# Performance work log

Measured on AMD Instinct MI355X. Metric: run time of the kernel, lower is better.

Reference implementation:

```python
import jax, jax.numpy as jnp
import numpy as np

K = 5       # kernel_size
UP = 2      # up_factor
EPS = 1e-5  # BatchNorm eps (eval mode)


def _conv(x, w, pad, dil=1):
    return jax.lax.conv_general_dilated(
        x, w, (1, 1), [(pad, pad), (pad, pad)], rhs_dilation=(dil, dil),
        dimension_numbers=('NCHW', 'OIHW', 'NCHW'))


def _bn(x, g, b, m, v):
    inv = g / jnp.sqrt(v + EPS)
    return x * inv[:, None, None] + (b - m * inv)[:, None, None]


def _bilinear(x, oh, ow):
    # torch F.interpolate(mode='bilinear', align_corners=False)
    N, C, H, W = x.shape
    def coords(out_s, in_s):
        s = in_s / out_s
        src = (jnp.arange(out_s, dtype=jnp.float32) + 0.5) * s - 0.5
        src = jnp.clip(src, 0.0, in_s - 1)
        i0 = jnp.floor(src).astype(jnp.int32)
        i1 = jnp.minimum(i0 + 1, in_s - 1)
        return i0, i1, src - i0
    y0, y1, wy = coords(oh, H)
    x0, x1, wx = coords(ow, W)
    g = lambda yi, xi: x[:, :, yi][:, :, :, xi]  # (N,C,oh,ow)
    top = g(y0, x0) * (1 - wx) + g(y0, x1) * wx
    bot = g(y1, x0) * (1 - wx) + g(y1, x1) * wx
    return top * (1 - wy)[:, None] + bot * wy[:, None]


def _unfold(x):
    # F.unfold(k=5, pad=2) reshaped to (N, C, K*K, H, W); channel-major (c, kh, kw)
    p = K // 2
    N, C, H, W = x.shape
    xp = jnp.pad(x, ((0, 0), (0, 0), (p, p), (p, p)))
    patches = [xp[:, :, i:i + H, j:j + W] for i in range(K) for j in range(K)]
    return jnp.stack(patches, axis=2)


def setup_inputs() -> dict:
    key = jax.random.key(0)
    ks = jax.random.split(key, 8)
    N, C, H, W = 2, 256, 48, 48
    Cc = C // 4
    Cout = 256
    d = {}
    d['x'] = jax.random.normal(ks[0], (N, C, H, W), dtype=jnp.float32)
    d['compress_w'] = jax.random.normal(ks[1], (Cc, C, 1, 1), dtype=jnp.float32) * 0.05
    d['g1'] = jnp.ones((Cc,), jnp.float32)
    d['b1'] = jnp.zeros((Cc,), jnp.float32)
    d['m1'] = jax.random.normal(ks[2], (Cc,), dtype=jnp.float32) * 0.1
    d['v1'] = jax.random.uniform(ks[3], (Cc,), minval=0.5, maxval=1.5, dtype=jnp.float32)
    d['ke1_w'] = jax.random.normal(ks[4], (Cc, Cc, 3, 3), dtype=jnp.float32) * 0.05
    d['gk'] = jnp.ones((Cc,), jnp.float32)
    d['bk'] = jnp.zeros((Cc,), jnp.float32)
    d['mk'] = jax.random.normal(ks[5], (Cc,), dtype=jnp.float32) * 0.1
    d['vk'] = jax.random.uniform(ks[6], (Cc,), minval=0.5, maxval=1.5, dtype=jnp.float32)
    d['ke2_w'] = jax.random.normal(ks[7], (UP * UP * K * K, Cc, 3, 3), dtype=jnp.float32) * 0.05
    d['proj_w'] = jax.random.normal(jax.random.fold_in(key, 10), (Cout, C, 1, 1), dtype=jnp.float32) * 0.05
    d['g2'] = jnp.ones((Cout,), jnp.float32)
    d['b2'] = jnp.zeros((Cout,), jnp.float32)
    d['m2'] = jax.random.normal(jax.random.fold_in(key, 11), (Cout,), dtype=jnp.float32) * 0.1
    d['v2'] = jax.random.uniform(jax.random.fold_in(key, 12), (Cout,), minval=0.5, maxval=1.5, dtype=jnp.float32)
    return d


def reference(x, compress_w, g1, b1, m1, v1, ke1_w, gk, bk, mk, vk, ke2_w,
              proj_w, g2, b2, m2, v2):
    N, C, H, W = x.shape
    oh, ow = H * UP, W * UP
    # kernel prediction branch
    comp = jax.nn.relu(_bn(_conv(x, compress_w, 0), g1, b1, m1, v1))
    k1 = jax.nn.relu(_bn(_conv(comp, ke1_w, 2, dil=2), gk, bk, mk, vk))
    kernel = _conv(k1, ke2_w, 1)                               # (N, UP^2*K^2, H, W)
    kernel = jax.nn.softmax(kernel.reshape(N, UP * UP, K * K, H, W), axis=2)
    # content reassembly
    x_up = jnp.repeat(jnp.repeat(x, UP, axis=2), UP, axis=3)
    x_unf = _unfold(x_up)                                      # (N, C, K^2, oh, ow)
    k_up = _bilinear(kernel.reshape(N, UP * UP * K * K, H, W), oh, ow)
    k_up = k_up.reshape(N, UP * UP, K * K, oh, ow)
    out = jnp.einsum('nckhw,nukhw->nuchw', x_unf, k_up)        # (N, UP^2, C, oh, ow)
    # view (N, UP^2*C, oh, ow) then pixel_shuffle(UP)
    out = out.reshape(N, UP * UP * C, oh, ow)
    out = out.reshape(N, C, UP, UP, oh, ow)
    out = out.transpose(0, 1, 4, 2, 5, 3).reshape(N, C, oh * UP, ow * UP)
    out = jax.nn.relu(_bn(_conv(out, proj_w, 0), g2, b2, m2, v2))
    return out
```

## Files before the change

kernel.cpp:

```cpp
#include <hip/hip_runtime.h>

#define EPSB 1e-5f

typedef __attribute__((ext_vector_type(8))) short bf16x8;
typedef __attribute__((ext_vector_type(4))) float f32x4;

__device__ __forceinline__ unsigned short f2b(float f) {
  union { float f; unsigned u; } cv; cv.f = f;
  unsigned r = cv.u + 0x7FFFu + ((cv.u >> 16) & 1u);
  return (unsigned short)(r >> 16);
}

__global__ __launch_bounds__(256) void k_compress(
    const float* __restrict__ x, const float* __restrict__ cw,
    const float* __restrict__ g1, const float* __restrict__ b1,
    const float* __restrict__ m1, const float* __restrict__ v1,
    const float* __restrict__ k1w, const float* __restrict__ k2w,
    const float* __restrict__ pw,
    unsigned short* __restrict__ comp_t, unsigned short* __restrict__ k1_t,
    unsigned short* __restrict__ pwb, unsigned short* __restrict__ wt1,
    unsigned short* __restrict__ wt2) {
  int bid = blockIdx.x, t = threadIdx.x;
  if (bid >= 96) {
    int u = (bid - 96) * 256 + t;
    if (u < 65536) {
      pwb[u] = f2b(pw[u]);
    } else if (u < 102400) {
      int a = u - 65536;
      int co = a / 576, k = a % 576, tap = k >> 6, ci = k & 63;
      wt1[a] = f2b(k1w[co * 576 + ci * 9 + tap]);
    } else if (u < 176128) {
      int c2 = u - 102400;
      int co = c2 / 576, k = c2 % 576, tap = k >> 6, ci = k & 63;
      wt2[c2] = (co < 100) ? f2b(k2w[co * 576 + ci * 9 + tap]) : (unsigned short)0;
    } else {
      int v = u - 176128;
      if (v < 25600) {
        int n = v / 12800, r = v % 12800;
        int bp = r >> 5, c32 = r & 31;
        int rr, cc;
        if (bp < 104) { rr = bp / 52; cc = bp % 52; }
        else if (bp >= 296) { rr = 50 + (bp - 296) / 52; cc = (bp - 296) % 52; }
        else { int q = bp - 104; rr = 2 + (q >> 2); int c4 = q & 3; cc = (c4 < 2) ? c4 : c4 + 48; }
        ((unsigned*)comp_t)[((size_t)n * 2704 + rr * 52 + cc) * 32 + c32] = 0u;
      } else if (v < 38144) {
        int j = v - 25600;
        int n = j / 6272, r = j % 6272;
        int bp = r >> 5, c32 = r & 31;
        int rr, cc;
        if (bp < 50) { rr = 0; cc = bp; }
        else if (bp >= 146) { rr = 49; cc = bp - 146; }
        else { int q = bp - 50; rr = 1 + (q >> 1); cc = (q & 1) * 49; }
        ((unsigned*)k1_t)[((size_t)n * 2500 + rr * 50 + cc) * 32 + c32] = 0u;
      }
    }
    return;
  }
  __shared__ __align__(16) unsigned short wlds[16384];
  __shared__ __align__(16) unsigned short xlds[12288];
  int n = bid / 48, y = bid % 48;
  for (int f = t; f < 16384; f += 256) {
    int co = f >> 8, ci = f & 255;
    int ba = (f * 2) ^ ((co & 7) << 4);
    *(unsigned short*)((char*)wlds + ba) = f2b(cw[f]);
  }
  const float* xrow = x + (size_t)n * 256 * 2304 + y * 48;
  for (int f = t; f < 12288; f += 256) {
    int ci = f / 48, px = f - ci * 48;
    int ba = ((px * 256 + ci) * 2) ^ ((px & 7) << 4);
    *(unsigned short*)((char*)xlds + ba) = f2b(xrow[(size_t)ci * 2304 + px]);
  }
  __syncthreads();
  int wid = t >> 6, l = t & 63, l15 = l & 15, lg = l >> 4;
  f32x4 acc[3];
  acc[0] = acc[1] = acc[2] = (f32x4){0.f, 0.f, 0.f, 0.f};
  int coA = wid * 16 + l15;
#pragma unroll
  for (int kbi = 0; kbi < 8; ++kbi) {
    int col = kbi * 32 + lg * 8;
    bf16x8 afr = *(const bf16x8*)((char*)wlds + (((coA * 256 + col) * 2) ^ ((coA & 7) << 4)));
#pragma unroll
    for (int nt = 0; nt < 3; ++nt) {
      int px = nt * 16 + l15;
      bf16x8 bfr = *(const bf16x8*)((char*)xlds + (((px * 256 + col) * 2) ^ ((px & 7) << 4)));
      acc[nt] = __builtin_amdgcn_mfma_f32_16x16x32_bf16(afr, bfr, acc[nt], 0, 0, 0);
    }
  }
  int co0 = wid * 16 + lg * 4;
  float s0 = g1[co0] / sqrtf(v1[co0] + EPSB);
  float s1 = g1[co0 + 1] / sqrtf(v1[co0 + 1] + EPSB);
  float s2 = g1[co0 + 2] / sqrtf(v1[co0 + 2] + EPSB);
  float s3 = g1[co0 + 3] / sqrtf(v1[co0 + 3] + EPSB);
  float d0 = b1[co0] - m1[co0] * s0;
  float d1 = b1[co0 + 1] - m1[co0 + 1] * s1;
  float d2 = b1[co0 + 2] - m1[co0 + 2] * s2;
  float d3 = b1[co0 + 3] - m1[co0 + 3] * s3;
  unsigned short* dst = comp_t + ((size_t)n * 2704 + (y + 2) * 52) * 64;
#pragma unroll
  for (int nt = 0; nt < 3; ++nt) {
    int px = nt * 16 + l15;
    ushort4 pk;
    pk.x = f2b(fmaxf(fmaf(acc[nt][0], s0, d0), 0.f));
    pk.y = f2b(fmaxf(fmaf(acc[nt][1], s1, d1), 0.f));
    pk.z = f2b(fmaxf(fmaf(acc[nt][2], s2, d2), 0.f));
    pk.w = f2b(fmaxf(fmaf(acc[nt][3], s3, d3), 0.f));
    *(ushort4*)&dst[(px + 2) * 64 + co0] = pk;
  }
}

__global__ __launch_bounds__(128) void k_ke1(
    const unsigned short* __restrict__ comp_t, const unsigned short* __restrict__ wt1,
    const float* __restrict__ gk, const float* __restrict__ bk,
    const float* __restrict__ mk, const float* __restrict__ vk,
    unsigned short* __restrict__ k1_t) {
  __shared__ unsigned short sA[16640];
  int bid = blockIdx.x, t = threadIdx.x;
  int n = bid / 96, rem = bid % 96;
  int y = rem >> 1, coh = rem & 1;
  const unsigned short* src = comp_t + ((size_t)n * 52 + y) * 52 * 64;
  for (int f = t; f < 2080; f += 128) {
    int g = f >> 3, ci0 = (f & 7) * 8;
    int cc = g % 52, rr = g / 52;
    bf16x8 vv = *(const bf16x8*)&src[(rr * 52 + cc) * 64 + ci0];
    int ba = (((rr * 52 + cc) * 64 + ci0) * 2) ^ ((cc & 7) << 4);
    *(bf16x8*)((char*)sA + ba) = vv;
  }
  __syncthreads();
  int wid = t >> 6, l = t & 63, l15 = l & 15, lg = l >> 4;
  f32x4 acc[3];
  acc[0] = acc[1] = acc[2] = (f32x4){0.f, 0.f, 0.f, 0.f};
  const unsigned short* arow = wt1 + (size_t)(coh * 32 + wid * 16 + l15) * 576;
#pragma unroll
  for (int kbi = 0; kbi < 18; ++kbi) {
    int tap = kbi >> 1;
    int ky = tap / 3, kx = tap % 3;
    int ci0 = (kbi & 1) * 32 + lg * 8;
    bf16x8 afr = *(const bf16x8*)&arow[kbi * 32 + lg * 8];
#pragma unroll
    for (int nt = 0; nt < 3; ++nt) {
      int col = nt * 16 + l15 + 2 * kx;
      int ba = (((2 * ky * 52 + col) * 64 + ci0) * 2) ^ ((col & 7) << 4);
      bf16x8 bfr = *(const bf16x8*)((char*)sA + ba);
      acc[nt] = __builtin_amdgcn_mfma_f32_16x16x32_bf16(afr, bfr, acc[nt], 0, 0, 0);
    }
  }
  unsigned short* dst = k1_t + ((size_t)n * 50 + (y + 1)) * 50 * 64;
  int co0 = coh * 32 + wid * 16 + lg * 4;
  float s0 = gk[co0] / sqrtf(vk[co0] + EPSB);
  float s1 = gk[co0 + 1] / sqrtf(vk[co0 + 1] + EPSB);
  float s2 = gk[co0 + 2] / sqrtf(vk[co0 + 2] + EPSB);
  float s3 = gk[co0 + 3] / sqrtf(vk[co0 + 3] + EPSB);
  float d0 = bk[co0] - mk[co0] * s0;
  float d1 = bk[co0 + 1] - mk[co0 + 1] * s1;
  float d2 = bk[co0 + 2] - mk[co0 + 2] * s2;
  float d3 = bk[co0 + 3] - mk[co0 + 3] * s3;
#pragma unroll
  for (int nt = 0; nt < 3; ++nt) {
    int px = nt * 16 + l15;
    ushort4 pk;
    pk.x = f2b(fmaxf(fmaf(acc[nt][0], s0, d0), 0.f));
    pk.y = f2b(fmaxf(fmaf(acc[nt][1], s1, d1), 0.f));
    pk.z = f2b(fmaxf(fmaf(acc[nt][2], s2, d2), 0.f));
    pk.w = f2b(fmaxf(fmaf(acc[nt][3], s3, d3), 0.f));
    *(ushort4*)&dst[(px + 1) * 64 + co0] = pk;
  }
}

__global__ __launch_bounds__(128) void k_ke2(
    const unsigned short* __restrict__ k1_t, const unsigned short* __restrict__ wt2,
    float* __restrict__ kern_t) {
  __shared__ unsigned short sA[9600];
  int bid = blockIdx.x, t = threadIdx.x;
  int n = bid / 96, rem = bid % 96;
  int y = rem >> 1, coh = rem & 1;
  const unsigned short* src = k1_t + ((size_t)n * 50 + y) * 50 * 64;
  for (int f = t; f < 1200; f += 128) {
    int g = f >> 3, ci0 = (f & 7) * 8;
    int cc = g % 50, rr = g / 50;
    bf16x8 vv = *(const bf16x8*)&src[(rr * 50 + cc) * 64 + ci0];
    int ba = (((rr * 50 + cc) * 64 + ci0) * 2) ^ ((cc & 7) << 4);
    *(bf16x8*)((char*)sA + ba) = vv;
  }
  __syncthreads();
  int wid = t >> 6, l = t & 63, l15 = l & 15, lg = l >> 4;
  f32x4 acc[2][3];
#pragma unroll
  for (int mi = 0; mi < 2; ++mi)
#pragma unroll
    for (int nt = 0; nt < 3; ++nt) acc[mi][nt] = (f32x4){0.f, 0.f, 0.f, 0.f};
#pragma unroll
  for (int kbi = 0; kbi < 18; ++kbi) {
    int tap = kbi >> 1;
    int ky = tap / 3, kx = tap % 3;
    int ci0 = (kbi & 1) * 32 + lg * 8;
    bf16x8 afr[2];
#pragma unroll
    for (int mi = 0; mi < 2; ++mi)
      afr[mi] = *(const bf16x8*)&wt2[(size_t)(coh * 64 + (wid * 2 + mi) * 16 + l15) * 576 + kbi * 32 + lg * 8];
#pragma unroll
    for (int nt = 0; nt < 3; ++nt) {
      int col = nt * 16 + l15 + kx;
      int ba = (((ky * 50 + col) * 64 + ci0) * 2) ^ ((col & 7) << 4);
      bf16x8 bfr = *(const bf16x8*)((char*)sA + ba);
      acc[0][nt] = __builtin_amdgcn_mfma_f32_16x16x32_bf16(afr[0], bfr, acc[0][nt], 0, 0, 0);
      acc[1][nt] = __builtin_amdgcn_mfma_f32_16x16x32_bf16(afr[1], bfr, acc[1][nt], 0, 0, 0);
    }
  }
#pragma unroll
  for (int mi = 0; mi < 2; ++mi) {
    int co0 = coh * 64 + (wid * 2 + mi) * 16 + lg * 4;
    if (co0 < 112) {
#pragma unroll
      for (int nt = 0; nt < 3; ++nt) {
        int px = nt * 16 + l15;
        float4 vv = {acc[mi][nt][0], acc[mi][nt][1], acc[mi][nt][2], acc[mi][nt][3]};
        *(float4*)&kern_t[((size_t)n * 2304 + y * 48 + px) * 112 + co0] = vv;
      }
    }
  }
}

__global__ __launch_bounds__(512, 4) void k_fused(
    const float* __restrict__ x, const float* __restrict__ kern_t,
    const unsigned short* __restrict__ pwb,
    const float* __restrict__ g2, const float* __restrict__ b2,
    const float* __restrict__ m2, const float* __restrict__ v2,
    float* __restrict__ out) {
  __shared__ __align__(16) char smem[76800];
  float* xls  = (float*)smem;
  float* w9s  = (float*)(smem + 35840);
  float* sb2s = (float*)(smem + 40448);
  unsigned short* finT = (unsigned short*)(smem + 44032);
  float* ks   = (float*)(smem + 44032);

  int blk = blockIdx.x;
  int n = blk / 288, r = blk % 288;
  int y48 = r / 6, xt = r % 6;
  int X0 = xt * 32, x480 = xt * 8;
  int t = threadIdx.x;

  if (t < 256) {
    float iv = g2[t] / sqrtf(v2[t] + EPSB);
    sb2s[t] = iv; sb2s[256 + t] = b2[t] - m2[t] * iv;
  }
  for (int f = t; f < 840; f += 512) {
    int slot = f / 280, rem = f % 280;
    int cx = rem / 28, c4 = rem % 28;
    int sy = min(max(y48 + slot - 1, 0), 47);
    int sx = min(max(x480 + cx - 1, 0), 47);
    float4 vv = *(const float4*)&kern_t[((size_t)n * 2304 + sy * 48 + sx) * 112 + c4 * 4];
    *(float4*)&ks[(slot * 10 + cx) * 112 + c4 * 4] = vv;
  }
  const float* xb = x + (size_t)n * 256 * 2304;
  for (int f = t; f < 8448; f += 512) {
    int c = f / 33, rc = f - c * 33;
    int ry = rc / 11, cx = rc - ry * 11;
    int sy = min(max(y48 + ry - 1, 0), 47);
    int sx = min(max(x480 + cx - 1, 0), 47);
    int slot = (c & 3) * 64 + (c >> 2);
    xls[slot * 35 + rc] = xb[(size_t)c * 2304 + sy * 48 + sx];
  }
  __syncthreads();

  {
    int s = t & 3, tri = t >> 2;
    int u = tri & 3, w2l = (tri >> 2) & 15, yhh = tri >> 6;
    int y96 = 2 * y48 + yhh;
    int w2 = xt * 16 + w2l;
    float syf = fminf(fmaxf(y96 * 0.5f - 0.25f, 0.f), 47.f);
    int y0 = (int)syf; float wy = syf - (float)y0; int y1 = min(y0 + 1, 47);
    float sxf = fminf(fmaxf(w2 * 0.5f - 0.25f, 0.f), 47.f);
    int x0 = (int)sxf; float wx = sxf - (float)x0; int x1 = min(x0 + 1, 47);
    int slr = ((s & 2) ? y1 : y0) - y48 + 1;
    int cxr = ((s & 1) ? x1 : x0) - x480 + 1;
    float wgt = ((s & 1) ? wx : 1.f - wx) * ((s & 2) ? wy : 1.f - wy);
    const float* p = &ks[(slr * 10 + cxr) * 112 + u * 25];
    float bl[25], mx = -3.4e38f;
#pragma unroll
    for (int k = 0; k < 25; ++k) { bl[k] = p[k]; mx = fmaxf(mx, bl[k]); }
    float sum = 0.f;
#pragma unroll
    for (int k = 0; k < 25; ++k) { bl[k] = __expf(bl[k] - mx); sum += bl[k]; }
    float rs = wgt / sum;
#pragma unroll
    for (int k = 0; k < 25; ++k) {
      bl[k] *= rs;
      bl[k] += __shfl_xor(bl[k], 1);
      bl[k] += __shfl_xor(bl[k], 2);
    }
    if (s == 0) {
#pragma unroll
      for (int kh = 0; kh < 5; ++kh) {
        bool vy = (unsigned)(y96 + kh - 2) < 96u;
#pragma unroll
        for (int kw = 0; kw < 5; ++kw) {
          bool vx = (unsigned)(w2 + kw - 2) < 96u;
          if (!(vy && vx)) bl[kh * 5 + kw] = 0.f;
        }
      }
      int py = yhh, px_ = w2l & 1;
      float cc0[5], cc1[5], cc2[5];
#pragma unroll
      for (int kh = 0; kh < 5; ++kh) {
        cc0[kh] = px_ ? bl[kh * 5 + 0] : bl[kh * 5 + 0] + bl[kh * 5 + 1];
        cc1[kh] = px_ ? bl[kh * 5 + 1] + bl[kh * 5 + 2] : bl[kh * 5 + 2] + bl[kh * 5 + 3];
        cc2[kh] = px_ ? bl[kh * 5 + 3] + bl[kh * 5 + 4] : bl[kh * 5 + 4];
      }
      float* op = &w9s[(yhh * 16 + w2l) * 36 + u * 9];
      op[0] = py ? cc0[0] : cc0[0] + cc0[1];
      op[1] = py ? cc1[0] : cc1[0] + cc1[1];
      op[2] = py ? cc2[0] : cc2[0] + cc2[1];
      op[3] = py ? cc0[1] + cc0[2] : cc0[2] + cc0[3];
      op[4] = py ? cc1[1] + cc1[2] : cc1[2] + cc1[3];
      op[5] = py ? cc2[1] + cc2[2] : cc2[2] + cc2[3];
      op[6] = py ? cc0[3] + cc0[4] : cc0[4];
      op[7] = py ? cc1[3] + cc1[4] : cc1[4];
      op[8] = py ? cc2[3] + cc2[4] : cc2[4];
    }
  }
  __syncthreads();

  int ci = t & 255, rY = t >> 8;
  int u = ci >> 6, ch = ci & 63;
  int cb = ci >> 3, crr = ci & 7;
  int wid = t >> 6, l = t & 63, l15 = l & 15, lg = l >> 4;
  const unsigned short* a0p = pwb + (size_t)(wid * 32 + l15) * 256;
  const unsigned short* a1p = a0p + 16 * 256;
  size_t outn = (size_t)n * 256 * 36864;
  int Ybase = 4 * y48;

#pragma unroll
  for (int c = 0; c < 2; ++c) {
    {
      const float* xc0 = &xls[((rY * 2 + 0) * 64 + ch) * 35];
      const float* xc1 = &xls[((rY * 2 + 1) * 64 + ch) * 35];
      float xw0[9], xw1[9];
#pragma unroll
      for (int ry = 0; ry < 3; ++ry)
#pragma unroll
        for (int cx = 0; cx < 3; ++cx) {
          xw0[ry * 3 + cx] = xc0[ry * 11 + cx];
          xw1[ry * 3 + cx] = xc1[ry * 11 + cx];
        }
#pragma unroll
      for (int j = 0; j < 16; ++j) {
        if (j >= 2 && (j & 1) == 0) {
          int nc = (j >> 1) + 2;
#pragma unroll
          for (int ry = 0; ry < 3; ++ry) {
            xw0[ry*3+0]=xw0[ry*3+1]; xw0[ry*3+1]=xw0[ry*3+2]; xw0[ry*3+2]=xc0[ry*11+nc];
            xw1[ry*3+0]=xw1[ry*3+1]; xw1[ry*3+1]=xw1[ry*3+2]; xw1[ry*3+2]=xc1[ry*11+nc];
          }
        }
        const float* wt = &w9s[(c * 16 + j) * 36 + u * 9];
        float a0 = 0.f, a1 = 0.f;
#pragma unroll
        for (int k9 = 0; k9 < 9; ++k9) {
          float wv = wt[k9];
          a0 = fmaf(xw0[k9], wv, a0);
          a1 = fmaf(xw1[k9], wv, a1);
        }
        int px0 = rY * 32 + 2 * j, px1 = px0 + 1;
        finT[px0 * 256 + ((cb ^ (px0 & 7)) * 8 + crr)] = f2b(a0);
        finT[px1 * 256 + ((cb ^ (px1 & 7)) * 8 + crr)] = f2b(a1);
      }
    }
    __syncthreads();

    f32x4 acc[2][4];
#pragma unroll
    for (int mi = 0; mi < 2; ++mi)
#pragma unroll
      for (int nt = 0; nt < 4; ++nt) acc[mi][nt] = (f32x4){0.f, 0.f, 0.f, 0.f};
#pragma unroll
    for (int kbi = 0; kbi < 8; ++kbi) {
      bf16x8 afr0 = *(const bf16x8*)&a0p[kbi * 32 + lg * 8];
      bf16x8 afr1 = *(const bf16x8*)&a1p[kbi * 32 + lg * 8];
      int cbk = kbi * 4 + lg;
#pragma unroll
      for (int nt = 0; nt < 4; ++nt) {
        int row = nt * 16 + l15;
        bf16x8 bfr = *(const bf16x8*)&finT[row * 256 + ((cbk ^ (row & 7)) * 8)];
        acc[0][nt] = __builtin_amdgcn_mfma_f32_16x16x32_bf16(afr0, bfr, acc[0][nt], 0, 0, 0);
        acc[1][nt] = __builtin_amdgcn_mfma_f32_16x16x32_bf16(afr1, bfr, acc[1][nt], 0, 0, 0);
      }
    }
#pragma unroll
    for (int mi = 0; mi < 2; ++mi) {
#pragma unroll
      for (int r4 = 0; r4 < 4; ++r4) {
        int o = (wid * 2 + mi) * 16 + lg * 4 + r4;
        float sc = sb2s[o], bi = sb2s[256 + o];
#pragma unroll
        for (int nt = 0; nt < 4; ++nt) {
          int px = nt * 16 + l15;
          int Yl = c * 2 + (px >> 5), Xl = px & 31;
          float val = fmaxf(fmaf(acc[mi][nt][r4], sc, bi), 0.f);
          out[outn + (size_t)o * 36864 + (size_t)(Ybase + Yl) * 192 + X0 + Xl] = val;
        }
      }
    }
    if (c == 0) __syncthreads();
  }
}

extern "C" void kernel_launch(void* const* d_in, const int* in_sizes, int n_in,
                              void* d_out, int out_size, void* d_ws, size_t ws_size,
                              hipStream_t stream) {
  const float* x   = (const float*)d_in[0];
  const float* cw  = (const float*)d_in[1];
  const float* g1  = (const float*)d_in[2];
  const float* b1  = (const float*)d_in[3];
  const float* m1  = (const float*)d_in[4];
  const float* v1  = (const float*)d_in[5];
  const float* k1w = (const float*)d_in[6];
  const float* gk  = (const float*)d_in[7];
  const float* bk  = (const float*)d_in[8];
  const float* mk  = (const float*)d_in[9];
  const float* vk  = (const float*)d_in[10];
  const float* k2w = (const float*)d_in[11];
  const float* pw  = (const float*)d_in[12];
  const float* g2  = (const float*)d_in[13];
  const float* b2  = (const float*)d_in[14];
  const float* m2  = (const float*)d_in[15];
  const float* v2  = (const float*)d_in[16];
  float* out = (float*)d_out;
  float* ws  = (float*)d_ws;

  unsigned short* comp_t = (unsigned short*)ws;
  unsigned short* k1_t   = (unsigned short*)(ws + 173056);
  float* kern_t = ws + 333056;
  unsigned short* pwb = (unsigned short*)(ws + 849152);
  unsigned short* wt1 = (unsigned short*)(ws + 881920);
  unsigned short* wt2 = (unsigned short*)(ws + 900352);

  k_compress<<<933, 256, 0, stream>>>(x, cw, g1, b1, m1, v1, k1w, k2w, pw,
                                      comp_t, k1_t, pwb, wt1, wt2);
  k_ke1<<<192, 128, 0, stream>>>(comp_t, wt1, gk, bk, mk, vk, k1_t);
  k_ke2<<<192, 128, 0, stream>>>(k1_t, wt2, kern_t);
  k_fused<<<576, 512, 0, stream>>>(x, kern_t, pwb, g2, b2, m2, v2, out);
}
```

Before: 185.9 us.

## Fuse ke1 and ke2 convolutions into main kernel with halo recompute

Removes the separate ke1 and ke2 kernels and their global intermediates. Each block of the fused kernel now computes the dilated 3x3 conv and the kernel-prediction conv for its own tile plus a halo from comp_t in shared memory, then proceeds to reassembly and projection. The x tile is also staged as bf16 instead of fp32 to reduce shared memory use. This saves two launches and global round trips, at the cost of redundant halo compute (each block recomputes overlapping k1 and kernel values) and lower precision on x.

```diff
diff --git a/kernel.cpp b/kernel.cpp
--- a/kernel.cpp
+++ b/kernel.cpp
@@ -9,6 +9,10 @@
   union { float f; unsigned u; } cv; cv.f = f;
   unsigned r = cv.u + 0x7FFFu + ((cv.u >> 16) & 1u);
   return (unsigned short)(r >> 16);
+}
+__device__ __forceinline__ float b2f(unsigned short v) {
+  union { unsigned u; float f; } cv; cv.u = ((unsigned)v) << 16;
+  return cv.f;
 }
 
 __global__ __launch_bounds__(256) void k_compress(
@@ -17,9 +21,8 @@
     const float* __restrict__ m1, const float* __restrict__ v1,
     const float* __restrict__ k1w, const float* __restrict__ k2w,
     const float* __restrict__ pw,
-    unsigned short* __restrict__ comp_t, unsigned short* __restrict__ k1_t,
-    unsigned short* __restrict__ pwb, unsigned short* __restrict__ wt1,
-    unsigned short* __restrict__ wt2) {
+    unsigned short* __restrict__ comp_t, unsigned short* __restrict__ pwb,
+    unsigned short* __restrict__ wt1, unsigned short* __restrict__ wt2) {
   int bid = blockIdx.x, t = threadIdx.x;
   if (bid >= 96) {
     int u = (bid - 96) * 256 + t;
@@ -43,15 +46,6 @@
         else if (bp >= 296) { rr = 50 + (bp - 296) / 52; cc = (bp - 296) % 52; }
         else { int q = bp - 104; rr = 2 + (q >> 2); int c4 = q & 3; cc = (c4 < 2) ? c4 : c4 + 48; }
         ((unsigned*)comp_t)[((size_t)n * 2704 + rr * 52 + cc) * 32 + c32] = 0u;
-      } else if (v < 38144) {
-        int j = v - 25600;
-        int n = j / 6272, r = j % 6272;
-        int bp = r >> 5, c32 = r & 31;
-        int rr, cc;
-        if (bp < 50) { rr = 0; cc = bp; }
-        else if (bp >= 146) { rr = 49; cc = bp - 146; }
-        else { int q = bp - 50; rr = 1 + (q >> 1); cc = (q & 1) * 49; }
-        ((unsigned*)k1_t)[((size_t)n * 2500 + rr * 50 + cc) * 32 + c32] = 0u;
       }
     }
     return;
@@ -60,7 +54,7 @@
   __shared__ __align__(16) unsigned short xlds[12288];
   int n = bid / 48, y = bid % 48;
   for (int f = t; f < 16384; f += 256) {
-    int co = f >> 8, ci = f & 255;
+    int co = f >> 8;
     int ba = (f * 2) ^ ((co & 7) << 4);
     *(unsigned short*)((char*)wlds + ba) = f2b(cw[f]);
   }
@@ -108,148 +102,51 @@
   }
 }
 
-__global__ __launch_bounds__(128) void k_ke1(
-    const unsigned short* __restrict__ comp_t, const unsigned short* __restrict__ wt1,
+__global__ __launch_bounds__(512, 4) void k_mega(
+    const float* __restrict__ x, const unsigned short* __restrict__ comp_t,
+    const unsigned short* __restrict__ wt1, const unsigned short* __restrict__ wt2,
+    const unsigned short* __restrict__ pwb,
     const float* __restrict__ gk, const float* __restrict__ bk,
     const float* __restrict__ mk, const float* __restrict__ vk,
-    unsigned short* __restrict__ k1_t) {
-  __shared__ unsigned short sA[16640];
-  int bid = blockIdx.x, t = threadIdx.x;
-  int n = bid / 96, rem = bid % 96;
-  int y = rem >> 1, coh = rem & 1;
-  const unsigned short* src = comp_t + ((size_t)n * 52 + y) * 52 * 64;
-  for (int f = t; f < 2080; f += 128) {
-    int g = f >> 3, ci0 = (f & 7) * 8;
-    int cc = g % 52, rr = g / 52;
-    bf16x8 vv = *(const bf16x8*)&src[(rr * 52 + cc) * 64 + ci0];
-    int ba = (((rr * 52 + cc) * 64 + ci0) * 2) ^ ((cc & 7) << 4);
-    *(bf16x8*)((char*)sA + ba) = vv;
-  }
-  __syncthreads();
-  int wid = t >> 6, l = t & 63, l15 = l & 15, lg = l >> 4;
-  f32x4 acc[3];
-  acc[0] = acc[1] = acc[2] = (f32x4){0.f, 0.f, 0.f, 0.f};
-  const unsigned short* arow = wt1 + (size_t)(coh * 32 + wid * 16 + l15) * 576;
-#pragma unroll
-  for (int kbi = 0; kbi < 18; ++kbi) {
-    int tap = kbi >> 1;
-    int ky = tap / 3, kx = tap % 3;
-    int ci0 = (kbi & 1) * 32 + lg * 8;
-    bf16x8 afr = *(const bf16x8*)&arow[kbi * 32 + lg * 8];
-#pragma unroll
-    for (int nt = 0; nt < 3; ++nt) {
-      int col = nt * 16 + l15 + 2 * kx;
-      int ba = (((2 * ky * 52 + col) * 64 + ci0) * 2) ^ ((col & 7) << 4);
-      bf16x8 bfr = *(const bf16x8*)((char*)sA + ba);
-      acc[nt] = __builtin_amdgcn_mfma_f32_16x16x32_bf16(afr, bfr, acc[nt], 0, 0, 0);
-    }
-  }
-  unsigned short* dst = k1_t + ((size_t)n * 50 + (y + 1)) * 50 * 64;
-  int co0 = coh * 32 + wid * 16 + lg * 4;
-  float s0 = gk[co0] / sqrtf(vk[co0] + EPSB);
-  float s1 = gk[co0 + 1] / sqrtf(vk[co0 + 1] + EPSB);
-  float s2 = gk[co0 + 2] / sqrtf(vk[co0 + 2] + EPSB);
-  float s3 = gk[co0 + 3] / sqrtf(vk[co0 + 3] + EPSB);
-  float d0 = bk[co0] - mk[co0] * s0;
-  float d1 = bk[co0 + 1] - mk[co0 + 1] * s1;
-  float d2 = bk[co0 + 2] - mk[co0 + 2] * s2;
-  float d3 = bk[co0 + 3] - mk[co0 + 3] * s3;
-#pragma unroll
-  for (int nt = 0; nt < 3; ++nt) {
-    int px = nt * 16 + l15;
-    ushort4 pk;
-    pk.x = f2b(fmaxf(fmaf(acc[nt][0], s0, d0), 0.f));
-    pk.y = f2b(fmaxf(fmaf(acc[nt][1], s1, d1), 0.f));
-    pk.z = f2b(fmaxf(fmaf(acc[nt][2], s2, d2), 0.f));
-    pk.w = f2b(fmaxf(fmaf(acc[nt][3], s3, d3), 0.f));
-    *(ushort4*)&dst[(px + 1) * 64 + co0] = pk;
-  }
-}
-
-__global__ __launch_bounds__(128) void k_ke2(
-    const unsigned short* __restrict__ k1_t, const unsigned short* __restrict__ wt2,
-    float* __restrict__ kern_t) {
-  __shared__ unsigned short sA[9600];
-  int bid = blockIdx.x, t = threadIdx.x;
-  int n = bid / 96, rem = bid % 96;
-  int y = rem >> 1, coh = rem & 1;
-  const unsigned short* src = k1_t + ((size_t)n * 50 + y) * 50 * 64;
-  for (int f = t; f < 1200; f += 128) {
-    int g = f >> 3, ci0 = (f & 7) * 8;
-    int cc = g % 50, rr = g / 50;
-    bf16x8 vv = *(const bf16x8*)&src[(rr * 50 + cc) * 64 + ci0];
-    int ba = (((rr * 50 + cc) * 64 + ci0) * 2) ^ ((cc & 7) << 4);
-    *(bf16x8*)((char*)sA + ba) = vv;
-  }
-  __syncthreads();
-  int wid = t >> 6, l = t & 63, l15 = l & 15, lg = l >> 4;
-  f32x4 acc[2][3];
-#pragma unroll
-  for (int mi = 0; mi < 2; ++mi)
-#pragma unroll
-    for (int nt = 0; nt < 3; ++nt) acc[mi][nt] = (f32x4){0.f, 0.f, 0.f, 0.f};
-#pragma unroll
-  for (int kbi = 0; kbi < 18; ++kbi) {
-    int tap = kbi >> 1;
-    int ky = tap / 3, kx = tap % 3;
-    int ci0 = (kbi & 1) * 32 + lg * 8;
-    bf16x8 afr[2];
-#pragma unroll
-    for (int mi = 0; mi < 2; ++mi)
-      afr[mi] = *(const bf16x8*)&wt2[(size_t)(coh * 64 + (wid * 2 + mi) * 16 + l15) * 576 + kbi * 32 + lg * 8];
-#pragma unroll
-    for (int nt = 0; nt < 3; ++nt) {
-      int col = nt * 16 + l15 + kx;
-      int ba = (((ky * 50 + col) * 64 + ci0) * 2) ^ ((col & 7) << 4);
-      bf16x8 bfr = *(const bf16x8*)((char*)sA + ba);
-      acc[0][nt] = __builtin_amdgcn_mfma_f32_16x16x32_bf16(afr[0], bfr, acc[0][nt], 0, 0, 0);
-      acc[1][nt] = __builtin_amdgcn_mfma_f32_16x16x32_bf16(afr[1], bfr, acc[1][nt], 0, 0, 0);
-    }
-  }
-#pragma unroll
-  for (int mi = 0; mi < 2; ++mi) {
-    int co0 = coh * 64 + (wid * 2 + mi) * 16 + lg * 4;
-    if (co0 < 112) {
-#pragma unroll
-      for (int nt = 0; nt < 3; ++nt) {
-        int px = nt * 16 + l15;
-        float4 vv = {acc[mi][nt][0], acc[mi][nt][1], acc[mi][nt][2], acc[mi][nt][3]};
-        *(float4*)&kern_t[((size_t)n * 2304 + y * 48 + px) * 112 + co0] = vv;
-      }
-    }
-  }
-}
-
-__global__ __launch_bounds__(512, 4) void k_fused(
-    const float* __restrict__ x, const float* __restrict__ kern_t,
-    const unsigned short* __restrict__ pwb,
     const float* __restrict__ g2, const float* __restrict__ b2,
     const float* __restrict__ m2, const float* __restrict__ v2,
     float* __restrict__ out) {
-  __shared__ __align__(16) char smem[76800];
-  float* xls  = (float*)smem;
-  float* w9s  = (float*)(smem + 35840);
-  float* sb2s = (float*)(smem + 40448);
-  unsigned short* finT = (unsigned short*)(smem + 44032);
-  float* ks   = (float*)(smem + 44032);
+  __shared__ __align__(16) char smem[66752];
+  unsigned short* xls_b = (unsigned short*)smem;
+  float* w9s   = (float*)(smem + 18944);
+  float* sb2s  = (float*)(smem + 23552);
+  float* sbk   = (float*)(smem + 25600);
+  char*  comp_sB = smem + 26112;
+  char*  k1_sB   = smem + 44544;
+  float* kern_s  = (float*)(smem + 52352);
+  unsigned short* finT = (unsigned short*)(smem + 26112);
 
   int blk = blockIdx.x;
   int n = blk / 288, r = blk % 288;
   int y48 = r / 6, xt = r % 6;
   int X0 = xt * 32, x480 = xt * 8;
   int t = threadIdx.x;
+  int wv = t >> 6, l = t & 63, l15 = l & 15, lg = l >> 4;
 
   if (t < 256) {
     float iv = g2[t] / sqrtf(v2[t] + EPSB);
     sb2s[t] = iv; sb2s[256 + t] = b2[t] - m2[t] * iv;
-  }
-  for (int f = t; f < 840; f += 512) {
-    int slot = f / 280, rem = f % 280;
-    int cx = rem / 28, c4 = rem % 28;
-    int sy = min(max(y48 + slot - 1, 0), 47);
-    int sx = min(max(x480 + cx - 1, 0), 47);
-    float4 vv = *(const float4*)&kern_t[((size_t)n * 2304 + sy * 48 + sx) * 112 + c4 * 4];
-    *(float4*)&ks[(slot * 10 + cx) * 112 + c4 * 4] = vv;
+  } else if (t < 320) {
+    int c = t - 256;
+    float iv = gk[c] / sqrtf(vk[c] + EPSB);
+    sbk[c] = iv; sbk[64 + c] = bk[c] - mk[c] * iv;
+  }
+  for (int f = t; f < 1152; f += 512) {
+    int ci0 = (f & 7) * 8;
+    int g = f >> 3;
+    int cc = g & 15, rr = g >> 4;
+    int pr = y48 - 2 + rr;
+    int pc = x480 - 2 + cc;
+    bf16x8 vv = (bf16x8){0, 0, 0, 0, 0, 0, 0, 0};
+    if ((unsigned)pr < 52u && (unsigned)pc < 52u)
+      vv = *(const bf16x8*)&comp_t[(((size_t)n * 52 + pr) * 52 + pc) * 64 + ci0];
+    int ba = ((rr * 16 + cc) * 64 + ci0) * 2 ^ ((cc & 7) << 4);
+    *(bf16x8*)(comp_sB + ba) = vv;
   }
   const float* xb = x + (size_t)n * 256 * 2304;
   for (int f = t; f < 8448; f += 512) {
@@ -258,7 +155,65 @@
     int sy = min(max(y48 + ry - 1, 0), 47);
     int sx = min(max(x480 + cx - 1, 0), 47);
     int slot = (c & 3) * 64 + (c >> 2);
-    xls[slot * 35 + rc] = xb[(size_t)c * 2304 + sy * 48 + sx];
+    xls_b[slot * 37 + rc] = f2b(xb[(size_t)c * 2304 + sy * 48 + sx]);
+  }
+  __syncthreads();
+
+  for (int tk = wv; tk < 16; tk += 8) {
+    int cotile = tk >> 2, pxtile = tk & 3;
+    int p = pxtile * 16 + l15;
+    int pcr = min(p, 59);
+    int rowp = pcr / 12, colp = pcr - rowp * 12;
+    f32x4 acc = (f32x4){0.f, 0.f, 0.f, 0.f};
+    const unsigned short* arow = wt1 + (size_t)(cotile * 16 + l15) * 576;
+#pragma unroll
+    for (int kbi = 0; kbi < 18; ++kbi) {
+      int tap = kbi >> 1;
+      int ky = tap / 3, kx = tap % 3;
+      int ci0 = (kbi & 1) * 32 + lg * 8;
+      bf16x8 afr = *(const bf16x8*)&arow[kbi * 32 + lg * 8];
+      int crow = rowp + 2 * ky, ccol = colp + 2 * kx;
+      int ba = ((crow * 16 + ccol) * 64 + ci0) * 2 ^ ((ccol & 7) << 4);
+      bf16x8 bfr = *(const bf16x8*)(comp_sB + ba);
+      acc = __builtin_amdgcn_mfma_f32_16x16x32_bf16(afr, bfr, acc, 0, 0, 0);
+    }
+    int co0 = cotile * 16 + lg * 4;
+    bool valid = (p < 60) && ((unsigned)(y48 - 2 + rowp) < 48u) && ((unsigned)(x480 - 2 + colp) < 48u);
+    int wslot = min(p, 60);
+    ushort4 pk;
+    pk.x = valid ? f2b(fmaxf(fmaf(acc[0], sbk[co0], sbk[64 + co0]), 0.f)) : (unsigned short)0;
+    pk.y = valid ? f2b(fmaxf(fmaf(acc[1], sbk[co0 + 1], sbk[64 + co0 + 1]), 0.f)) : (unsigned short)0;
+    pk.z = valid ? f2b(fmaxf(fmaf(acc[2], sbk[co0 + 2], sbk[64 + co0 + 2]), 0.f)) : (unsigned short)0;
+    pk.w = valid ? f2b(fmaxf(fmaf(acc[3], sbk[co0 + 3], sbk[64 + co0 + 3]), 0.f)) : (unsigned short)0;
+    *(ushort4*)(k1_sB + (((wslot * 64 + co0) * 2) ^ ((wslot & 7) << 4))) = pk;
+  }
+  __syncthreads();
+
+  for (int tk = wv; tk < 14; tk += 8) {
+    int cotile = tk % 7, pxtile = tk / 7;
+    int p = pxtile * 16 + l15;
+    int pcr = min(p, 29);
+    int s = pcr / 10, cx = pcr - s * 10;
+    int gr = min(max(y48 - 1 + s, 0), 47);
+    int gc = min(max(x480 - 1 + cx, 0), 47);
+    int lrb = gr - y48 + 1, lcb = gc - x480 + 1;
+    f32x4 acc = (f32x4){0.f, 0.f, 0.f, 0.f};
+    const unsigned short* arow = wt2 + (size_t)(cotile * 16 + l15) * 576;
+#pragma unroll
+    for (int kbi = 0; kbi < 18; ++kbi) {
+      int tap = kbi >> 1;
+      int ky = tap / 3, kx = tap % 3;
+      int ci0 = (kbi & 1) * 32 + lg * 8;
+      bf16x8 afr = *(const bf16x8*)&arow[kbi * 32 + lg * 8];
+      int pk1 = (lrb + ky) * 12 + (lcb + kx);
+      int ba = ((pk1 * 64 + ci0) * 2) ^ ((pk1 & 7) << 4);
+      bf16x8 bfr = *(const bf16x8*)(k1_sB + ba);
+      acc = __builtin_amdgcn_mfma_f32_16x16x32_bf16(afr, bfr, acc, 0, 0, 0);
+    }
+    int co0 = cotile * 16 + lg * 4;
+    int wslot = min(p, 30);
+    float4 vv = {acc[0], acc[1], acc[2], acc[3]};
+    *(float4*)&kern_s[wslot * 116 + co0] = vv;
   }
   __syncthreads();
 
@@ -274,7 +229,7 @@
     int slr = ((s & 2) ? y1 : y0) - y48 + 1;
     int cxr = ((s & 1) ? x1 : x0) - x480 + 1;
     float wgt = ((s & 1) ? wx : 1.f - wx) * ((s & 2) ? wy : 1.f - wy);
-    const float* p = &ks[(slr * 10 + cxr) * 112 + u * 25];
+    const float* p = &kern_s[(slr * 10 + cxr) * 116 + u * 25];
     float bl[25], mx = -3.4e38f;
 #pragma unroll
     for (int k = 0; k < 25; ++k) { bl[k] = p[k]; mx = fmaxf(mx, bl[k]); }
@@ -323,8 +278,7 @@
   int ci = t & 255, rY = t >> 8;
   int u = ci >> 6, ch = ci & 63;
   int cb = ci >> 3, crr = ci & 7;
-  int wid = t >> 6, l = t & 63, l15 = l & 15, lg = l >> 4;
-  const unsigned short* a0p = pwb + (size_t)(wid * 32 + l15) * 256;
+  const unsigned short* a0p = pwb + (size_t)(wv * 32 + l15) * 256;
   const unsigned short* a1p = a0p + 16 * 256;
   size_t outn = (size_t)n * 256 * 36864;
   int Ybase = 4 * y48;
@@ -332,15 +286,15 @@
 #pragma unroll
   for (int c = 0; c < 2; ++c) {
     {
-      const float* xc0 = &xls[((rY * 2 + 0) * 64 + ch) * 35];
-      const float* xc1 = &xls[((rY * 2 + 1) * 64 + ch) * 35];
+      const unsigned short* xc0 = &xls_b[((rY * 2 + 0) * 64 + ch) * 37];
+      const unsigned short* xc1 = &xls_b[((rY * 2 + 1) * 64 + ch) * 37];
       float xw0[9], xw1[9];
 #pragma unroll
       for (int ry = 0; ry < 3; ++ry)
 #pragma unroll
         for (int cx = 0; cx < 3; ++cx) {
-          xw0[ry * 3 + cx] = xc0[ry * 11 + cx];
-          xw1[ry * 3 + cx] = xc1[ry * 11 + cx];
+          xw0[ry * 3 + cx] = b2f(xc0[ry * 11 + cx]);
+          xw1[ry * 3 + cx] = b2f(xc1[ry * 11 + cx]);
         }
 #pragma unroll
       for (int j = 0; j < 16; ++j) {
@@ -348,17 +302,17 @@
           int nc = (j >> 1) + 2;
 #pragma unroll
           for (int ry = 0; ry < 3; ++ry) {
-            xw0[ry*3+0]=xw0[ry*3+1]; xw0[ry*3+1]=xw0[ry*3+2]; xw0[ry*3+2]=xc0[ry*11+nc];
-            xw1[ry*3+0]=xw1[ry*3+1]; xw1[ry*3+1]=xw1[ry*3+2]; xw1[ry*3+2]=xc1[ry*11+nc];
+            xw0[ry*3+0]=xw0[ry*3+1]; xw0[ry*3+1]=xw0[ry*3+2]; xw0[ry*3+2]=b2f(xc0[ry*11+nc]);
+            xw1[ry*3+0]=xw1[ry*3+1]; xw1[ry*3+1]=xw1[ry*3+2]; xw1[ry*3+2]=b2f(xc1[ry*11+nc]);
           }
         }
         const float* wt = &w9s[(c * 16 + j) * 36 + u * 9];
         float a0 = 0.f, a1 = 0.f;
 #pragma unroll
         for (int k9 = 0; k9 < 9; ++k9) {
-          float wv = wt[k9];
-          a0 = fmaf(xw0[k9], wv, a0);
-          a1 = fmaf(xw1[k9], wv, a1);
+          float wvv = wt[k9];
+          a0 = fmaf(xw0[k9], wvv, a0);
+          a1 = fmaf(xw1[k9], wvv, a1);
         }
         int px0 = rY * 32 + 2 * j, px1 = px0 + 1;
         finT[px0 * 256 + ((cb ^ (px0 & 7)) * 8 + crr)] = f2b(a0);
@@ -389,7 +343,7 @@
     for (int mi = 0; mi < 2; ++mi) {
 #pragma unroll
       for (int r4 = 0; r4 < 4; ++r4) {
-        int o = (wid * 2 + mi) * 16 + lg * 4 + r4;
+        int o = (wv * 2 + mi) * 16 + lg * 4 + r4;
         float sc = sb2s[o], bi = sb2s[256 + o];
 #pragma unroll
         for (int nt = 0; nt < 4; ++nt) {
@@ -428,15 +382,12 @@
   float* ws  = (float*)d_ws;
 
   unsigned short* comp_t = (unsigned short*)ws;
-  unsigned short* k1_t   = (unsigned short*)(ws + 173056);
-  float* kern_t = ws + 333056;
-  unsigned short* pwb = (unsigned short*)(ws + 849152);
-  unsigned short* wt1 = (unsigned short*)(ws + 881920);
-  unsigned short* wt2 = (unsigned short*)(ws + 900352);
-
-  k_compress<<<933, 256, 0, stream>>>(x, cw, g1, b1, m1, v1, k1w, k2w, pw,
-                                      comp_t, k1_t, pwb, wt1, wt2);
-  k_ke1<<<192, 128, 0, stream>>>(comp_t, wt1, gk, bk, mk, vk, k1_t);
-  k_ke2<<<192, 128, 0, stream>>>(k1_t, wt2, kern_t);
-  k_fused<<<576, 512, 0, stream>>>(x, kern_t, pwb, g2, b2, m2, v2, out);
-}
+  unsigned short* pwb = (unsigned short*)(ws + 173056);
+  unsigned short* wt1 = (unsigned short*)(ws + 205824);
+  unsigned short* wt2 = (unsigned short*)(ws + 224256);
+
+  k_compress<<<884, 256, 0, stream>>>(x, cw, g1, b1, m1, v1, k1w, k2w, pw,
+                                      comp_t, pwb, wt1, wt2);
+  k_mega<<<576, 512, 0, stream>>>(x, comp_t, wt1, wt2, pwb,
+                                  gk, bk, mk, vk, g2, b2, m2, v2, out);
+}
```

After: 208.9 us. 12.3% more time.
